# Kernel optimization log

Hardware: AMD Instinct MI355X
Metric: run time of the kernel (lower is better)

Reference implementation:

```python
import jax, jax.numpy as jnp
import numpy as np

B = 16384
IN = 1024
H = 1024
LN_EPS = 1e-5


def setup_inputs() -> dict:
    key = jax.random.key(0)
    ks = jax.random.split(key, 8)
    # Five gate Linears fused into one weight [IN+H, 5H] (order: f, i, o, c, m)
    scale = 1.0 / np.sqrt(IN + H)
    W = jax.random.uniform(ks[0], (IN + H, 5 * H), jnp.float32, -scale, scale)
    b = jax.random.uniform(ks[1], (5 * H,), jnp.float32, -scale, scale)
    return {
        "x": jax.random.normal(ks[2], (B, IN), jnp.float32),
        "h_prev": jax.random.normal(ks[3], (B, H), jnp.float32),
        "c_prev": jax.random.normal(ks[4], (B, H), jnp.float32),
        "W": W,
        "b": b,
        "ln_gamma": jnp.ones((H,), jnp.float32),
        "ln_beta": jnp.zeros((H,), jnp.float32),
        "retention": jnp.full((H,), 0.9, jnp.float32),
    }


def _layernorm(z, gamma, beta):
    mu = jnp.mean(z, axis=-1, keepdims=True)
    var = jnp.var(z, axis=-1, keepdims=True)
    return (z - mu) * jax.lax.rsqrt(var + LN_EPS) * gamma + beta


def reference(x, h_prev, c_prev, W, b, ln_gamma, ln_beta, retention):
    combined = jnp.concatenate([x, h_prev], axis=-1)        # [B, IN+H]
    gates = combined @ W + b                                # [B, 5H] fused GEMM
    f_pre, i_pre, o_pre, c_pre_act, m_pre = jnp.split(gates, 5, axis=-1)
    f_gate = jax.nn.sigmoid(f_pre)
    i_gate = jax.nn.sigmoid(i_pre)
    o_gate = jax.nn.sigmoid(o_pre)
    c_cand = jnp.tanh(c_pre_act)
    m_gate = jax.nn.sigmoid(m_pre)
    c_new = f_gate * c_prev + i_gate * c_cand
    c_new = c_new * retention + (1.0 - retention) * c_prev
    c_new = m_gate * c_new + (1.0 - m_gate) * c_prev
    # exp(ln)/(1+exp(ln)) == sigmoid(layernorm(o_gate))
    o_exp = jax.nn.sigmoid(_layernorm(o_gate, ln_gamma, ln_beta))
    h_new = o_exp * jnp.tanh(c_new)
    return h_new, c_new
```

## Files before the change

kernel.cpp:

```cpp
#include <hip/hip_runtime.h>
#include <math.h>


typedef unsigned short u16;
typedef unsigned int   u32;
typedef short  short8 __attribute__((ext_vector_type(8)));
typedef float  f32x4  __attribute__((ext_vector_type(4)));
typedef u16    u16x4  __attribute__((ext_vector_type(4)));
typedef u32    u32x4  __attribute__((ext_vector_type(4)));

#define B_ROWS 16384
#define K_DIM  2048
#define N_DIM  5120
#define H_DIM  1024

__device__ __forceinline__ float b2f(u16 u) {
    u32 v = ((u32)u) << 16;
    return __uint_as_float(v);
}
__device__ __forceinline__ u16 f2b(float f) {
    u32 x = __float_as_uint(f);
    u32 r = (x + 0x7fffu + ((x >> 16) & 1u)) >> 16;
    return (u16)r;
}
__device__ __forceinline__ float sigm(float v) {
    return 1.f / (1.f + __expf(-v));
}
__device__ __forceinline__ float tanh_fast(float v) {
    v = fminf(fmaxf(v, -15.f), 15.f);
    float e = __expf(-2.f * v);
    return (1.f - e) / (1.f + e);
}

__global__ __launch_bounds__(256) void convert_A(const float* __restrict__ x,
                                                 const float* __restrict__ h,
                                                 u16* __restrict__ A) {
    size_t idx = ((size_t)blockIdx.x * 256 + threadIdx.x) * 8;
    int row = (int)(idx >> 11);
    int col = (int)(idx & 2047);
    int srcCol = (col & ~63) | (((((col >> 3) & 7) ^ (row & 7))) << 3);
    const float* src = (srcCol < 1024) ? (x + (size_t)row * 1024 + srcCol)
                                       : (h + (size_t)row * 1024 + (srcCol - 1024));
    f32x4 v0 = *(const f32x4*)src;
    f32x4 v1 = *(const f32x4*)(src + 4);
    u32x4 w;
    w.x = (u32)f2b(v0.x) | ((u32)f2b(v0.y) << 16);
    w.y = (u32)f2b(v0.z) | ((u32)f2b(v0.w) << 16);
    w.z = (u32)f2b(v1.x) | ((u32)f2b(v1.y) << 16);
    w.w = (u32)f2b(v1.z) | ((u32)f2b(v1.w) << 16);
    *(u32x4*)(A + idx) = w;
}

__global__ __launch_bounds__(256) void convert_W(const float* __restrict__ W,
                                                 u16* __restrict__ Wt) {
    __shared__ float tile[64][33];
    const int t  = threadIdx.x;
    const int tx = t & 31;
    const int ty = t >> 5;
    const int n0 = blockIdx.x * 32;
    const int k0 = blockIdx.y * 64;
#pragma unroll
    for (int i = 0; i < 8; ++i)
        tile[ty + 8 * i][tx] = W[(size_t)(k0 + ty + 8 * i) * N_DIM + n0 + tx];
    __syncthreads();
    const int n = t >> 3;
    const int s = t & 7;
    const int g = s ^ (n & 7);
    u32x4 w;
    w.x = (u32)f2b(tile[g * 8 + 0][n]) | ((u32)f2b(tile[g * 8 + 1][n]) << 16);
    w.y = (u32)f2b(tile[g * 8 + 2][n]) | ((u32)f2b(tile[g * 8 + 3][n]) << 16);
    w.z = (u32)f2b(tile[g * 8 + 4][n]) | ((u32)f2b(tile[g * 8 + 5][n]) << 16);
    w.w = (u32)f2b(tile[g * 8 + 6][n]) | ((u32)f2b(tile[g * 8 + 7][n]) << 16);
    *(u32x4*)(Wt + (size_t)(n0 + n) * K_DIM + k0 + s * 8) = w;
}

#define BK 64

__device__ __forceinline__ void gld_lds16(const void* g, void* l) {
    __builtin_amdgcn_global_load_lds(
        (const __attribute__((address_space(1))) void*)g,
        (__attribute__((address_space(3))) void*)l, 16, 0, 0);
}

#define AU(s, h) ((s) * 16384 + (h) * 8192)
#define BU(s, h) (32768 + (s) * 16384 + (h) * 8192)

#define BAR() do { __builtin_amdgcn_sched_barrier(0);                         \
                   __builtin_amdgcn_s_barrier();                              \
                   __builtin_amdgcn_sched_barrier(0); } while (0)
#define LGKM0() do { asm volatile("s_waitcnt lgkmcnt(0)" ::: "memory");       \
                     __builtin_amdgcn_sched_barrier(0); } while (0)
#define VM4() asm volatile("s_waitcnt vmcnt(4)" ::: "memory")

__global__ __launch_bounds__(512, 2) void gemm_gates(const u16* __restrict__ A,
                                                     const u16* __restrict__ Bt,
                                                     const float* __restrict__ bias,
                                                     u16* __restrict__ gates) {
    __shared__ u16 lds[65536];

    const int t = threadIdx.x;
    const int bid = blockIdx.x;
    const int swz = (bid & 7) * 160 + (bid >> 3);
    const int m0 = (swz & 63) << 8;
    const int n0 = (swz >> 6) << 8;

    const int l   = t & 63;
    const int wid = t >> 6;
    const int wr  = wid >> 2;
    const int wc  = wid & 3;
    const int lr  = l & 15;
    const int lh  = l >> 4;
    const int z   = lr & 7;
    const int sA0 = (lh ^ z) * 8;

    const int tb = t >> 3;
    const u16* aBase = A  + (size_t)(m0 + tb) * K_DIM + (t & 7) * 8;
    const u16* bBase = Bt + (size_t)(n0 + (tb & 31) + (tb >> 5) * 64) * K_DIM
                          + (t & 7) * 8;
    const int dOff = t * 8;

    f32x4 acc[8][4] = {};
    short8 afN[4][2], afC[4][2], bf0[2][2], bf1[2][2];

#define STAGE_A(s, h, OFF) do {                                               \
    gld_lds16(aBase + (size_t)((h) * 64) * K_DIM + (OFF),                     \
              &lds[AU(s, h) + dOff]);                                         \
    gld_lds16(aBase + (size_t)((h) * 64 + 128) * K_DIM + (OFF),               \
              &lds[AU(s, h) + 4096 + dOff]);                                  \
} while (0)
#define STAGE_B(s, h, OFF) do {                                               \
    gld_lds16(bBase + (size_t)((h) * 32) * K_DIM + (OFF),                     \
              &lds[BU(s, h) + dOff]);                                         \
    gld_lds16(bBase + (size_t)((h) * 32 + 128) * K_DIM + (OFF),               \
              &lds[BU(s, h) + 4096 + dOff]);                                  \
} while (0)

#define RD_AFX(dst, s, q) do {                                                \
    _Pragma("unroll") for (int m = 0; m < 4; ++m) {                           \
        const int u_ = AU(s, q) + (wr * 64 + m * 16 + lr) * 64;               \
        dst[m][0] = *(const short8*)&lds[u_ + sA0];                           \
        dst[m][1] = *(const short8*)&lds[u_ + (sA0 ^ 32)];                    \
    }                                                                         \
} while (0)
#define RD_BF(dst, s, h) do {                                                 \
    _Pragma("unroll") for (int n = 0; n < 2; ++n) {                           \
        const int u_ = BU(s, h) + (wc * 32 + n * 16 + lr) * 64;               \
        dst[n][0] = *(const short8*)&lds[u_ + sA0];                           \
        dst[n][1] = *(const short8*)&lds[u_ + (sA0 ^ 32)];                    \
    }                                                                         \
} while (0)

#define MFMA16(AF, q, nh, BF) do {                                            \
    __builtin_amdgcn_s_setprio(1);                                            \
    _Pragma("unroll") for (int sk = 0; sk < 2; ++sk)                          \
    _Pragma("unroll") for (int m = 0; m < 4; ++m)                             \
    _Pragma("unroll") for (int n = 0; n < 2; ++n)                             \
        acc[(q) * 4 + m][(nh) * 2 + n] =                                      \
            __builtin_amdgcn_mfma_f32_16x16x32_bf16(                          \
                AF[m][sk], BF[n][sk], acc[(q) * 4 + m][(nh) * 2 + n], 0, 0, 0);\
    __builtin_amdgcn_s_setprio(0);                                            \
} while (0)

    STAGE_A(0, 0, 0); STAGE_B(0, 0, 0); STAGE_B(0, 1, 0); STAGE_A(0, 1, 0);
    asm volatile("s_waitcnt vmcnt(0)" ::: "memory");
    BAR();
    RD_AFX(afN, 0, 0);

#pragma unroll 1
    for (int kt = 0; kt < 32; ++kt) {
        const int s  = kt & 1;
        const int sp = s ^ 1;
        const int OFF = (kt + 1) * BK;
        RD_BF(bf0, s, 0); STAGE_A(sp, 0, OFF);
        BAR(); LGKM0(); MFMA16(afN, 0, 0, bf0); VM4(); BAR();
        RD_BF(bf1, s, 1); STAGE_B(sp, 0, OFF);
        BAR(); LGKM0(); MFMA16(afN, 0, 1, bf1); VM4(); BAR();
        RD_AFX(afC, s, 1); STAGE_B(sp, 1, OFF);
        BAR(); LGKM0(); MFMA16(afC, 1, 1, bf1); VM4(); BAR();
        RD_AFX(afN, sp, 0); STAGE_A(sp, 1, OFF);
        BAR(); MFMA16(afC, 1, 0, bf0); VM4(); BAR();
    }
#undef STAGE_A
#undef STAGE_B

    asm volatile("s_waitcnt vmcnt(0)" ::: "memory");

    const int grp = n0 >> 10;
#pragma unroll
    for (int ni = 0; ni < 4; ++ni) {
        int col = n0 + wc * 64 + ni * 16 + lr;
        float bv = bias[col];
#pragma unroll
        for (int q = 0; q < 2; ++q) {
#pragma unroll
            for (int m = 0; m < 4; ++m) {
#pragma unroll
                for (int j = 0; j < 4; ++j) {
                    int row = m0 + wr * 128 + q * 64 + m * 16 + lh * 4 + j;
                    float v = acc[q * 4 + m][ni][j] + bv;
                    float g = (grp == 3) ? tanh_fast(v) : sigm(v);
                    gates[(size_t)row * N_DIM + col] = f2b(g);
                }
            }
        }
    }
#undef RD_AFX
#undef RD_BF
#undef MFMA16
}

__global__ __launch_bounds__(256) void fuse_out(const u16* __restrict__ gates,
                                                const float* __restrict__ c_prev,
                                                const float* __restrict__ ret,
                                                const float* __restrict__ gamma,
                                                const float* __restrict__ beta,
                                                float* __restrict__ out) {
    const int r = blockIdx.x;
    const int t = threadIdx.x;
    const u16* g = gates + (size_t)r * N_DIM;
    const int j0 = t * 4;

    u16x4 ov = *(const u16x4*)(g + 2048 + j0);
    float o0 = b2f(ov.x), o1 = b2f(ov.y), o2 = b2f(ov.z), o3 = b2f(ov.w);
    float s1 = o0 + o1 + o2 + o3;
    float s2 = o0 * o0 + o1 * o1 + o2 * o2 + o3 * o3;
#pragma unroll
    for (int off = 32; off; off >>= 1) {
        s1 += __shfl_xor(s1, off, 64);
        s2 += __shfl_xor(s2, off, 64);
    }
    __shared__ float red[8];
    if ((t & 63) == 0) { red[t >> 6] = s1; red[4 + (t >> 6)] = s2; }
    __syncthreads();
    float S1 = red[0] + red[1] + red[2] + red[3];
    float S2 = red[4] + red[5] + red[6] + red[7];
    float mu   = S1 * (1.f / 1024.f);
    float var  = S2 * (1.f / 1024.f) - mu * mu;
    float rstd = rsqrtf(var + 1e-5f);

    u16x4 fv = *(const u16x4*)(g + j0);
    u16x4 iv = *(const u16x4*)(g + 1024 + j0);
    u16x4 cv = *(const u16x4*)(g + 3072 + j0);
    u16x4 mv = *(const u16x4*)(g + 4096 + j0);
    f32x4 cp = *(const f32x4*)(c_prev + (size_t)r * H_DIM + j0);
    f32x4 rt = *(const f32x4*)(ret + j0);
    f32x4 gm = *(const f32x4*)(gamma + j0);
    f32x4 bt = *(const f32x4*)(beta + j0);

    float of[4] = {o0, o1, o2, o3};
    u16 fa[4] = {fv.x, fv.y, fv.z, fv.w};
    u16 ia[4] = {iv.x, iv.y, iv.z, iv.w};
    u16 ca[4] = {cv.x, cv.y, cv.z, cv.w};
    u16 ma[4] = {mv.x, mv.y, mv.z, mv.w};

    f32x4 hout, cout;
#pragma unroll
    for (int i = 0; i < 4; ++i) {
        float f = b2f(fa[i]), ig = b2f(ia[i]), cc = b2f(ca[i]), m = b2f(ma[i]);
        float cpv = cp[i], rv = rt[i];
        float c1 = f * cpv + ig * cc;
        float c2 = c1 * rv + (1.f - rv) * cpv;
        float cn = m * c2 + (1.f - m) * cpv;
        float ln = (of[i] - mu) * rstd * gm[i] + bt[i];
        float oe = sigm(ln);
        float hn = oe * tanh_fast(cn);
        hout[i] = hn;
        cout[i] = cn;
    }
    *(f32x4*)(out + (size_t)r * H_DIM + j0) = hout;
    *(f32x4*)(out + (size_t)B_ROWS * H_DIM + (size_t)r * H_DIM + j0) = cout;
}

extern "C" void kernel_launch(void* const* d_in, const int* in_sizes, int n_in,
                              void* d_out, int out_size, void* d_ws, size_t ws_size,
                              hipStream_t stream) {
    const float* x      = (const float*)d_in[0];
    const float* h_prev = (const float*)d_in[1];
    const float* c_prev = (const float*)d_in[2];
    const float* W      = (const float*)d_in[3];
    const float* bias   = (const float*)d_in[4];
    const float* gamma  = (const float*)d_in[5];
    const float* beta   = (const float*)d_in[6];
    const float* ret    = (const float*)d_in[7];
    float* out = (float*)d_out;

    u16* Abuf  = (u16*)d_ws;
    u16* Wt    = Abuf + (size_t)B_ROWS * K_DIM;
    u16* gates = Wt + (size_t)N_DIM * K_DIM;

    convert_A<<<(B_ROWS * K_DIM / 8) / 256, 256, 0, stream>>>(x, h_prev, Abuf);
    convert_W<<<dim3(N_DIM / 32, K_DIM / 64), 256, 0, stream>>>(W, Wt);
    gemm_gates<<<(B_ROWS / 256) * (N_DIM / 256), 512, 0, stream>>>(Abuf, Wt, bias, gates);
    fuse_out<<<B_ROWS, 256, 0, stream>>>(gates, c_prev, ret, gamma, beta, out);
}
```

Before: 482.5 us.

## Restructure GEMM main loop to prefetch A two stages ahead with fewer waits

Reorders the K-loop pipeline so the first A half-tile is prefetched two iterations ahead into the current buffer once it has been consumed, while B and the second A half load one stage ahead. The vmcnt waits are relaxed to fewer, looser points, and the sched_barrier fences around most s_barriers are removed so the compiler can interleave more freely. The goal is more memory latency hidden behind MFMA work. The risk is subtle LDS read/write hazards, since a buffer is overwritten in the same iteration it is read, and the looser waits may expose stalls.

```diff
diff --git a/kernel.cpp b/kernel.cpp
--- a/kernel.cpp
+++ b/kernel.cpp
@@ -85,12 +85,12 @@
 #define AU(s, h) ((s) * 16384 + (h) * 8192)
 #define BU(s, h) (32768 + (s) * 16384 + (h) * 8192)
 
-#define BAR() do { __builtin_amdgcn_sched_barrier(0);                         \
-                   __builtin_amdgcn_s_barrier();                              \
-                   __builtin_amdgcn_sched_barrier(0); } while (0)
+#define SB0()   __builtin_amdgcn_sched_barrier(0)
+#define SBAR()  __builtin_amdgcn_s_barrier()
 #define LGKM0() do { asm volatile("s_waitcnt lgkmcnt(0)" ::: "memory");       \
-                     __builtin_amdgcn_sched_barrier(0); } while (0)
-#define VM4() asm volatile("s_waitcnt vmcnt(4)" ::: "memory")
+                     SB0(); } while (0)
+#define VM6()   asm volatile("s_waitcnt vmcnt(6)" ::: "memory")
+#define VM4()   asm volatile("s_waitcnt vmcnt(4)" ::: "memory")
 
 __global__ __launch_bounds__(512, 2) void gemm_gates(const u16* __restrict__ A,
                                                      const u16* __restrict__ Bt,
@@ -120,7 +120,7 @@
     const int dOff = t * 8;
 
     f32x4 acc[8][4] = {};
-    short8 afN[4][2], afC[4][2], bf0[2][2], bf1[2][2];
+    short8 af0[4][2], af1[4][2], bf0[2][2], bf1[2][2];
 
 #define STAGE_A(s, h, OFF) do {                                               \
     gld_lds16(aBase + (size_t)((h) * 64) * K_DIM + (OFF),                     \
@@ -162,23 +162,30 @@
 } while (0)
 
     STAGE_A(0, 0, 0); STAGE_B(0, 0, 0); STAGE_B(0, 1, 0); STAGE_A(0, 1, 0);
-    asm volatile("s_waitcnt vmcnt(0)" ::: "memory");
-    BAR();
-    RD_AFX(afN, 0, 0);
+    STAGE_A(1, 0, BK);
+    VM4();
+    SBAR(); SB0();
 
 #pragma unroll 1
     for (int kt = 0; kt < 32; ++kt) {
         const int s  = kt & 1;
         const int sp = s ^ 1;
-        const int OFF = (kt + 1) * BK;
-        RD_BF(bf0, s, 0); STAGE_A(sp, 0, OFF);
-        BAR(); LGKM0(); MFMA16(afN, 0, 0, bf0); VM4(); BAR();
-        RD_BF(bf1, s, 1); STAGE_B(sp, 0, OFF);
-        BAR(); LGKM0(); MFMA16(afN, 0, 1, bf1); VM4(); BAR();
-        RD_AFX(afC, s, 1); STAGE_B(sp, 1, OFF);
-        BAR(); LGKM0(); MFMA16(afC, 1, 1, bf1); VM4(); BAR();
-        RD_AFX(afN, sp, 0); STAGE_A(sp, 1, OFF);
-        BAR(); MFMA16(afC, 1, 0, bf0); VM4(); BAR();
+        const int OFF1 = (kt + 1) * BK;
+        const int OFF2 = (kt + 2) * BK;
+        RD_AFX(af0, s, 0); RD_BF(bf0, s, 0); STAGE_B(sp, 0, OFF1);
+        SBAR(); LGKM0(); MFMA16(af0, 0, 0, bf0);
+        SBAR();
+        RD_BF(bf1, s, 1); STAGE_B(sp, 1, OFF1);
+        SBAR(); LGKM0(); MFMA16(af0, 0, 1, bf1);
+        VM6();
+        SBAR(); SB0();
+        RD_AFX(af1, s, 1); STAGE_A(sp, 1, OFF1);
+        SBAR(); LGKM0(); MFMA16(af1, 1, 1, bf1);
+        SBAR();
+        STAGE_A(s, 0, OFF2);
+        SBAR(); MFMA16(af1, 1, 0, bf0);
+        VM4();
+        SBAR(); SB0();
     }
 #undef STAGE_A
 #undef STAGE_B
```

Result: no change. 491.5 us (+1.9%).
